# Kernel optimization log

Measured on AMD Instinct MI355X. Metric: run time of the kernel, lower is better.

Reference implementation:

```python
import jax, jax.numpy as jnp
import numpy as np

N_NODES = 100000
N_EDGES = 1700000


def _build_csr(rng, n, e):
    row = rng.integers(0, n, size=e).astype(np.int64)
    col = rng.integers(0, n, size=e).astype(np.int32)
    order = np.argsort(row, kind='stable')
    row = row[order]
    col = col[order]
    rowptr = np.searchsorted(row, np.arange(n + 1)).astype(np.int32)
    return rowptr, col


def setup_inputs() -> dict:
    key = jax.random.key(0)
    k1, k2, k3, k4 = jax.random.split(key, 4)
    rng = np.random.default_rng(0)
    rowptr, colind = _build_csr(rng, N_NODES, N_EDGES)
    F_in, H, C = 256, 128, 16
    return {
        'x': jax.random.normal(k1, (N_NODES, F_in), dtype=jnp.float32),
        'edge_weight': jax.random.uniform(k2, (N_EDGES,), dtype=jnp.float32) + 0.5,
        'W1': jax.random.normal(k3, (F_in, H), dtype=jnp.float32) * (1.0 / np.sqrt(F_in)),
        'b1': jnp.zeros((H,), dtype=jnp.float32),
        'W2': jax.random.normal(k4, (H, C), dtype=jnp.float32) * (1.0 / np.sqrt(H)),
        'b2': jnp.zeros((C,), dtype=jnp.float32),
        'rowptr': jnp.asarray(rowptr),
        'colind': jnp.asarray(colind),
    }


def _rowids_from_rowptr(rowptr, n_edges):
    # CSR rowptr -> per-nnz row index, jit-friendly
    return (jnp.searchsorted(rowptr, jnp.arange(n_edges, dtype=rowptr.dtype), side='right') - 1).astype(jnp.int32)


def reference(x, edge_weight, W1, b1, W2, b2, rowptr, colind):
    n = x.shape[0]
    e = colind.shape[0]
    row = _rowids_from_rowptr(rowptr, e)
    col = colind

    # GCN symmetric normalization: D^-1/2 A D^-1/2 (cached=True -> shared by both layers)
    deg = jax.ops.segment_sum(edge_weight, row, num_segments=n)
    dinv = jnp.where(deg > 0, jax.lax.rsqrt(deg), 0.0)
    w = dinv[row] * edge_weight * dinv[col]

    def gcn_layer(h, W, b):
        h = h @ W                                   # [n, d_out]
        # SpMM: out[r] = sum_e w[e] * h[col[e]]
        msg = w[:, None] * h[col]                   # [e, d_out] gather
        return jax.ops.segment_sum(msg, row, num_segments=n) + b

    h = jax.nn.relu(gcn_layer(x, W1, b1))
    # dropout is identity in eval mode
    out = gcn_layer(h, W2, b2)
    return jax.nn.log_softmax(out, axis=1)
```

## Files before the change

### kernel.cpp

```cpp
#include <hip/hip_runtime.h>
#include <hip/hip_bf16.h>

#define F_IN 256
#define HDIM 128
#define CDIM 16

typedef unsigned short u16;
typedef unsigned int u32;

typedef __attribute__((ext_vector_type(8))) short bf16x8;
typedef __attribute__((ext_vector_type(4))) float f32x4;

__device__ __forceinline__ float bf2f(u32 v) {
    u32 u = v << 16;
    float f;
    __builtin_memcpy(&f, &u, 4);
    return f;
}
__device__ __forceinline__ u16 f2bf(float f) {
    u32 u;
    __builtin_memcpy(&u, &f, 4);
    u32 r = (u + 0x7FFFu + ((u >> 16) & 1u)) >> 16;
    return (u16)r;
}
__device__ __forceinline__ u32 pack2(float lo, float hi) {
    return ((u32)f2bf(hi) << 16) | (u32)f2bf(lo);
}

__global__ void k_dinv(const float* __restrict__ ew, const int* __restrict__ rowptr,
                       float* __restrict__ dinv, int n) {
    int r = blockIdx.x * blockDim.x + threadIdx.x;
    if (r >= n) return;
    int s = rowptr[r], e = rowptr[r + 1];
    float acc = 0.f;
    for (int i = s; i < e; i++) acc += ew[i];
    dinv[r] = (acc > 0.f) ? rsqrtf(acc) : 0.f;
}

__global__ void k_w(const float* __restrict__ ew, const int* __restrict__ rowptr,
                    const int* __restrict__ col, const float* __restrict__ dinv,
                    float* __restrict__ wn, int n) {
    int r = blockIdx.x * blockDim.x + threadIdx.x;
    if (r >= n) return;
    float dr = dinv[r];
    int s = rowptr[r], e = rowptr[r + 1];
    for (int i = s; i < e; i++) wn[i] = dr * ew[i] * dinv[col[i]];
}

__global__ void k_prepw1(const float* __restrict__ W1, u16* __restrict__ W1T) {
    int idx = blockIdx.x * blockDim.x + threadIdx.x;
    if (idx >= HDIM * F_IN) return;
    int f = idx >> 8;
    int k = idx & 255;
    W1T[idx] = f2bf(W1[(size_t)k * HDIM + f]);
}

__global__ __launch_bounds__(512, 4) void k_gemm1(const float* __restrict__ x,
                                                  const u16* __restrict__ W1T,
                                                  u16* __restrict__ T1, int n) {
    __shared__ u16 Bs[HDIM * F_IN];

    int tid = threadIdx.x;
#pragma unroll
    for (int it = 0; it < 8; it++) {
        int o16 = it * 512 + tid;
        u32 o = (u32)o16 * 16;
        u32 swz = o ^ (((o >> 9) & 7u) << 4);
        uint4 v = ((const uint4*)W1T)[o16];
        *(uint4*)((char*)Bs + swz) = v;
    }
    __syncthreads();

    int wave = tid >> 6;
    int lane = tid & 63;
    int lr = lane & 15;
    int kg = lane >> 4;
    int r0 = blockIdx.x * 256 + wave * 32;
    if (r0 >= n) return;

    f32x4 acc[2][8];
#pragma unroll
    for (int rg = 0; rg < 2; rg++)
#pragma unroll
        for (int ct = 0; ct < 8; ct++) acc[rg][ct] = (f32x4){0.f, 0.f, 0.f, 0.f};

    int rowc[2];
#pragma unroll
    for (int rg = 0; rg < 2; rg++) {
        int row = r0 + rg * 16 + lr;
        rowc[rg] = row < n ? row : (n - 1);
    }

#pragma unroll
    for (int kk = 0; kk < F_IN / 32; kk++) {
        bf16x8 afrag[2];
#pragma unroll
        for (int rg = 0; rg < 2; rg++) {
            const float4* ap = (const float4*)(x + (size_t)rowc[rg] * F_IN + kg * 8 + kk * 32);
            float4 alo = ap[0];
            float4 ahi = ap[1];
            afrag[rg][0] = (short)f2bf(alo.x); afrag[rg][1] = (short)f2bf(alo.y);
            afrag[rg][2] = (short)f2bf(alo.z); afrag[rg][3] = (short)f2bf(alo.w);
            afrag[rg][4] = (short)f2bf(ahi.x); afrag[rg][5] = (short)f2bf(ahi.y);
            afrag[rg][6] = (short)f2bf(ahi.z); afrag[rg][7] = (short)f2bf(ahi.w);
        }
#pragma unroll
        for (int ct = 0; ct < 8; ct++) {
            u32 a = (u32)(ct * 16 + lr) * (F_IN * 2) + (u32)kg * 16 + (u32)kk * 64;
            u32 aswz = a ^ (((a >> 9) & 7u) << 4);
            bf16x8 bfrag = *(const bf16x8*)((const char*)Bs + aswz);
#pragma unroll
            for (int rg = 0; rg < 2; rg++)
                acc[rg][ct] = __builtin_amdgcn_mfma_f32_16x16x32_bf16(afrag[rg], bfrag, acc[rg][ct], 0, 0, 0);
        }
    }

#pragma unroll
    for (int rg = 0; rg < 2; rg++) {
        int rbase = r0 + rg * 16 + kg * 4;
#pragma unroll
        for (int ct = 0; ct < 8; ct++) {
#pragma unroll
            for (int i = 0; i < 4; i++) {
                int row = rbase + i;
                if (row < n)
                    T1[(size_t)row * HDIM + ct * 16 + lr] = f2bf(acc[rg][ct][i]);
            }
        }
    }
}

__global__ __launch_bounds__(256) void k_spmm1(const u16* __restrict__ T1,
                                               const float* __restrict__ wn,
                                               const int* __restrict__ rowptr,
                                               const int* __restrict__ col,
                                               const float* __restrict__ b1,
                                               u16* __restrict__ H, int n) {
    int wave = threadIdx.x >> 6;
    int lane = threadIdx.x & 63;
    int r = blockIdx.x * 4 + wave;
    if (r >= n) return;
    int es = lane >> 4;
    int fl = lane & 15;

    int s = rowptr[r], e = rowptr[r + 1];
    float a[8];
#pragma unroll
    for (int j = 0; j < 8; j++) a[j] = 0.f;

    int i = s + es;
    for (; i + 4 < e; i += 8) {
        float w0 = wn[i];
        int c0 = col[i];
        float w1 = wn[i + 4];
        int c1 = col[i + 4];
        uint4 p0 = *(const uint4*)(T1 + (size_t)c0 * HDIM + fl * 8);
        uint4 p1 = *(const uint4*)(T1 + (size_t)c1 * HDIM + fl * 8);
        a[0] += w0 * bf2f(p0.x & 0xFFFFu); a[1] += w0 * bf2f(p0.x >> 16);
        a[2] += w0 * bf2f(p0.y & 0xFFFFu); a[3] += w0 * bf2f(p0.y >> 16);
        a[4] += w0 * bf2f(p0.z & 0xFFFFu); a[5] += w0 * bf2f(p0.z >> 16);
        a[6] += w0 * bf2f(p0.w & 0xFFFFu); a[7] += w0 * bf2f(p0.w >> 16);
        a[0] += w1 * bf2f(p1.x & 0xFFFFu); a[1] += w1 * bf2f(p1.x >> 16);
        a[2] += w1 * bf2f(p1.y & 0xFFFFu); a[3] += w1 * bf2f(p1.y >> 16);
        a[4] += w1 * bf2f(p1.z & 0xFFFFu); a[5] += w1 * bf2f(p1.z >> 16);
        a[6] += w1 * bf2f(p1.w & 0xFFFFu); a[7] += w1 * bf2f(p1.w >> 16);
    }
    if (i < e) {
        float w0 = wn[i];
        int c0 = col[i];
        uint4 p0 = *(const uint4*)(T1 + (size_t)c0 * HDIM + fl * 8);
        a[0] += w0 * bf2f(p0.x & 0xFFFFu); a[1] += w0 * bf2f(p0.x >> 16);
        a[2] += w0 * bf2f(p0.y & 0xFFFFu); a[3] += w0 * bf2f(p0.y >> 16);
        a[4] += w0 * bf2f(p0.z & 0xFFFFu); a[5] += w0 * bf2f(p0.z >> 16);
        a[6] += w0 * bf2f(p0.w & 0xFFFFu); a[7] += w0 * bf2f(p0.w >> 16);
    }

#pragma unroll
    for (int j = 0; j < 8; j++) {
        a[j] += __shfl_xor(a[j], 16);
        a[j] += __shfl_xor(a[j], 32);
    }

    if (es == 0) {
        const float4* bb = (const float4*)(b1 + fl * 8);
        float4 blo = bb[0], bhi = bb[1];
        float v0 = a[0] + blo.x, v1 = a[1] + blo.y;
        float v2 = a[2] + blo.z, v3 = a[3] + blo.w;
        float v4 = a[4] + bhi.x, v5 = a[5] + bhi.y;
        float v6 = a[6] + bhi.z, v7 = a[7] + bhi.w;
        v0 = v0 > 0.f ? v0 : 0.f; v1 = v1 > 0.f ? v1 : 0.f;
        v2 = v2 > 0.f ? v2 : 0.f; v3 = v3 > 0.f ? v3 : 0.f;
        v4 = v4 > 0.f ? v4 : 0.f; v5 = v5 > 0.f ? v5 : 0.f;
        v6 = v6 > 0.f ? v6 : 0.f; v7 = v7 > 0.f ? v7 : 0.f;
        uint4 o;
        o.x = pack2(v0, v1); o.y = pack2(v2, v3);
        o.z = pack2(v4, v5); o.w = pack2(v6, v7);
        *(uint4*)(H + (size_t)r * HDIM + fl * 8) = o;
    }
}

__global__ __launch_bounds__(256) void k_gemm2(const u16* __restrict__ H,
                                               const float* __restrict__ W2,
                                               float* __restrict__ U, int n) {
    int rl = threadIdx.x >> 4;
    int f = threadIdx.x & 15;
    int row = blockIdx.x * 16 + rl;
    if (row >= n) return;
    const u32* hr = (const u32*)(H + (size_t)row * HDIM);
    float acc = 0.f;
    for (int k2 = 0; k2 < HDIM / 2; k2++) {
        u32 pr = hr[k2];
        float h0 = bf2f(pr & 0xFFFFu);
        float h1 = bf2f(pr >> 16);
        acc += h0 * W2[(size_t)(k2 * 2) * CDIM + f];
        acc += h1 * W2[(size_t)(k2 * 2 + 1) * CDIM + f];
    }
    U[(size_t)row * CDIM + f] = acc;
}

__global__ __launch_bounds__(256) void k_out(const float* __restrict__ U,
                                             const float* __restrict__ wn,
                                             const int* __restrict__ rowptr,
                                             const int* __restrict__ col,
                                             const float* __restrict__ b2,
                                             float* __restrict__ out, int n) {
    int wave = threadIdx.x >> 6;
    int lane = threadIdx.x & 63;
    int r = blockIdx.x * 4 + wave;
    if (r >= n) return;
    int es = lane >> 4;
    int f = lane & 15;
    int s = rowptr[r], e = rowptr[r + 1];
    float acc = 0.f;
    int i = s + es;
    for (; i + 4 < e; i += 8) {
        float w0 = wn[i];
        int c0 = col[i];
        float w1 = wn[i + 4];
        int c1 = col[i + 4];
        acc += w0 * U[(size_t)c0 * CDIM + f];
        acc += w1 * U[(size_t)c1 * CDIM + f];
    }
    if (i < e) {
        acc += wn[i] * U[(size_t)col[i] * CDIM + f];
    }
    acc += __shfl_xor(acc, 16);
    acc += __shfl_xor(acc, 32);
    float v = acc + b2[f];
    float m = v;
    for (int d = 1; d < 16; d <<= 1) m = fmaxf(m, __shfl_xor(m, d));
    float ex = __expf(v - m);
    float ss = ex;
    for (int d = 1; d < 16; d <<= 1) ss += __shfl_xor(ss, d);
    float res = v - m - __logf(ss);
    if (es == 0) out[(size_t)r * CDIM + f] = res;
}

extern "C" void kernel_launch(void* const* d_in, const int* in_sizes, int n_in,
                              void* d_out, int out_size, void* d_ws, size_t ws_size,
                              hipStream_t stream) {
    const float* x      = (const float*)d_in[0];
    const float* ew     = (const float*)d_in[1];
    const float* W1     = (const float*)d_in[2];
    const float* b1     = (const float*)d_in[3];
    const float* W2     = (const float*)d_in[4];
    const float* b2     = (const float*)d_in[5];
    const int*   rowptr = (const int*)d_in[6];
    const int*   colind = (const int*)d_in[7];

    int n = in_sizes[6] - 1;
    int E = in_sizes[7];

    auto align256 = [](size_t v) { return (v + 255) & ~(size_t)255; };
    char* p = (char*)d_ws;
    float* dinv = (float*)p; p += align256((size_t)n * 4);
    float* wn   = (float*)p; p += align256((size_t)E * 4);
    u16*   T1   = (u16*)p;   p += align256((size_t)n * HDIM * 2);
    u16*   H    = (u16*)p;   p += align256((size_t)n * HDIM * 2);
    float* U    = (float*)p; p += align256((size_t)n * CDIM * 4);
    u16*   W1T  = (u16*)p;   p += align256((size_t)HDIM * F_IN * 2);
    float* out  = (float*)d_out;

    k_dinv<<<(n + 255) / 256, 256, 0, stream>>>(ew, rowptr, dinv, n);
    k_w<<<(n + 255) / 256, 256, 0, stream>>>(ew, rowptr, colind, dinv, wn, n);
    k_prepw1<<<(HDIM * F_IN + 255) / 256, 256, 0, stream>>>(W1, W1T);

    k_gemm1<<<(n + 255) / 256, 512, 0, stream>>>(x, W1T, T1, n);

    k_spmm1<<<(n + 3) / 4, 256, 0, stream>>>(T1, wn, rowptr, colind, b1, H, n);
    k_gemm2<<<(n + 15) / 16, 256, 0, stream>>>(H, W2, U, n);
    k_out<<<(n + 3) / 4, 256, 0, stream>>>(U, wn, rowptr, colind, b2, out, n);
}
```

Measured before the change: 198.7 us.

## Use packed bf16 convert, deepen SpMM1 unroll, widen k_out gather lanes

Replaces the software fp32-to-bf16 rounding with the hardware v_cvt_pk_bf16_f32 instruction in the GEMM1 A-fragment conversion, the T1 store and the H store. The layer-1 SpMM loop is unrolled to four gathers per lane in flight, to raise memory-level parallelism. The layer-2 gather kernel now assigns 8 edge slots of 8 lanes, each lane loading a float2, so more edges are gathered in parallel per row. The log-softmax reductions are shortened to match. The inline asm depends on the target supporting that instruction, and the deeper unroll raises register use.

```diff
diff --git a/kernel.cpp b/kernel.cpp
--- a/kernel.cpp
+++ b/kernel.cpp
@@ -23,8 +23,10 @@
     u32 r = (u + 0x7FFFu + ((u >> 16) & 1u)) >> 16;
     return (u16)r;
 }
-__device__ __forceinline__ u32 pack2(float lo, float hi) {
-    return ((u32)f2bf(hi) << 16) | (u32)f2bf(lo);
+__device__ __forceinline__ u32 cvtpk(float lo, float hi) {
+    u32 r;
+    asm("v_cvt_pk_bf16_f32 %0, %1, %2" : "=v"(r) : "v"(lo), "v"(hi));
+    return r;
 }
 
 __global__ void k_dinv(const float* __restrict__ ew, const int* __restrict__ rowptr,
@@ -99,10 +101,12 @@
             const float4* ap = (const float4*)(x + (size_t)rowc[rg] * F_IN + kg * 8 + kk * 32);
             float4 alo = ap[0];
             float4 ahi = ap[1];
-            afrag[rg][0] = (short)f2bf(alo.x); afrag[rg][1] = (short)f2bf(alo.y);
-            afrag[rg][2] = (short)f2bf(alo.z); afrag[rg][3] = (short)f2bf(alo.w);
-            afrag[rg][4] = (short)f2bf(ahi.x); afrag[rg][5] = (short)f2bf(ahi.y);
-            afrag[rg][6] = (short)f2bf(ahi.z); afrag[rg][7] = (short)f2bf(ahi.w);
+            u32 q0 = cvtpk(alo.x, alo.y);
+            u32 q1 = cvtpk(alo.z, alo.w);
+            u32 q2 = cvtpk(ahi.x, ahi.y);
+            u32 q3 = cvtpk(ahi.z, ahi.w);
+            u32 qa[4] = {q0, q1, q2, q3};
+            __builtin_memcpy(&afrag[rg], qa, 16);
         }
 #pragma unroll
         for (int ct = 0; ct < 8; ct++) {
@@ -121,10 +125,12 @@
 #pragma unroll
         for (int ct = 0; ct < 8; ct++) {
 #pragma unroll
-            for (int i = 0; i < 4; i++) {
-                int row = rbase + i;
-                if (row < n)
-                    T1[(size_t)row * HDIM + ct * 16 + lr] = f2bf(acc[rg][ct][i]);
+            for (int i = 0; i < 4; i += 2) {
+                u32 q = cvtpk(acc[rg][ct][i], acc[rg][ct][i + 1]);
+                int row0 = rbase + i;
+                int row1 = rbase + i + 1;
+                if (row0 < n) T1[(size_t)row0 * HDIM + ct * 16 + lr] = (u16)(q & 0xFFFFu);
+                if (row1 < n) T1[(size_t)row1 * HDIM + ct * 16 + lr] = (u16)(q >> 16);
             }
         }
     }
@@ -148,32 +154,35 @@
 #pragma unroll
     for (int j = 0; j < 8; j++) a[j] = 0.f;
 
+#define ACCUM(w_, p_) do { \
+        a[0] += (w_) * bf2f((p_).x & 0xFFFFu); a[1] += (w_) * bf2f((p_).x >> 16); \
+        a[2] += (w_) * bf2f((p_).y & 0xFFFFu); a[3] += (w_) * bf2f((p_).y >> 16); \
+        a[4] += (w_) * bf2f((p_).z & 0xFFFFu); a[5] += (w_) * bf2f((p_).z >> 16); \
+        a[6] += (w_) * bf2f((p_).w & 0xFFFFu); a[7] += (w_) * bf2f((p_).w >> 16); \
+    } while (0)
+
     int i = s + es;
-    for (; i + 4 < e; i += 8) {
-        float w0 = wn[i];
-        int c0 = col[i];
-        float w1 = wn[i + 4];
-        int c1 = col[i + 4];
+    for (; i + 12 < e; i += 16) {
+        float w0 = wn[i];      int c0 = col[i];
+        float w1 = wn[i + 4];  int c1 = col[i + 4];
+        float w2 = wn[i + 8];  int c2 = col[i + 8];
+        float w3 = wn[i + 12]; int c3 = col[i + 12];
         uint4 p0 = *(const uint4*)(T1 + (size_t)c0 * HDIM + fl * 8);
         uint4 p1 = *(const uint4*)(T1 + (size_t)c1 * HDIM + fl * 8);
-        a[0] += w0 * bf2f(p0.x & 0xFFFFu); a[1] += w0 * bf2f(p0.x >> 16);
-        a[2] += w0 * bf2f(p0.y & 0xFFFFu); a[3] += w0 * bf2f(p0.y >> 16);
-        a[4] += w0 * bf2f(p0.z & 0xFFFFu); a[5] += w0 * bf2f(p0.z >> 16);
-        a[6] += w0 * bf2f(p0.w & 0xFFFFu); a[7] += w0 * bf2f(p0.w >> 16);
-        a[0] += w1 * bf2f(p1.x & 0xFFFFu); a[1] += w1 * bf2f(p1.x >> 16);
-        a[2] += w1 * bf2f(p1.y & 0xFFFFu); a[3] += w1 * bf2f(p1.y >> 16);
-        a[4] += w1 * bf2f(p1.z & 0xFFFFu); a[5] += w1 * bf2f(p1.z >> 16);
-        a[6] += w1 * bf2f(p1.w & 0xFFFFu); a[7] += w1 * bf2f(p1.w >> 16);
-    }
-    if (i < e) {
+        uint4 p2 = *(const uint4*)(T1 + (size_t)c2 * HDIM + fl * 8);
+        uint4 p3 = *(const uint4*)(T1 + (size_t)c3 * HDIM + fl * 8);
+        ACCUM(w0, p0);
+        ACCUM(w1, p1);
+        ACCUM(w2, p2);
+        ACCUM(w3, p3);
+    }
+    for (; i < e; i += 4) {
         float w0 = wn[i];
         int c0 = col[i];
         uint4 p0 = *(const uint4*)(T1 + (size_t)c0 * HDIM + fl * 8);
-        a[0] += w0 * bf2f(p0.x & 0xFFFFu); a[1] += w0 * bf2f(p0.x >> 16);
-        a[2] += w0 * bf2f(p0.y & 0xFFFFu); a[3] += w0 * bf2f(p0.y >> 16);
-        a[4] += w0 * bf2f(p0.z & 0xFFFFu); a[5] += w0 * bf2f(p0.z >> 16);
-        a[6] += w0 * bf2f(p0.w & 0xFFFFu); a[7] += w0 * bf2f(p0.w >> 16);
-    }
+        ACCUM(w0, p0);
+    }
+#undef ACCUM
 
 #pragma unroll
     for (int j = 0; j < 8; j++) {
@@ -193,8 +202,8 @@
         v4 = v4 > 0.f ? v4 : 0.f; v5 = v5 > 0.f ? v5 : 0.f;
         v6 = v6 > 0.f ? v6 : 0.f; v7 = v7 > 0.f ? v7 : 0.f;
         uint4 o;
-        o.x = pack2(v0, v1); o.y = pack2(v2, v3);
-        o.z = pack2(v4, v5); o.w = pack2(v6, v7);
+        o.x = cvtpk(v0, v1); o.y = cvtpk(v2, v3);
+        o.z = cvtpk(v4, v5); o.w = cvtpk(v6, v7);
         *(uint4*)(H + (size_t)r * HDIM + fl * 8) = o;
     }
 }
@@ -228,32 +237,48 @@
     int lane = threadIdx.x & 63;
     int r = blockIdx.x * 4 + wave;
     if (r >= n) return;
-    int es = lane >> 4;
-    int f = lane & 15;
+    int es = lane >> 3;
+    int fl = lane & 7;
     int s = rowptr[r], e = rowptr[r + 1];
-    float acc = 0.f;
+    float a0 = 0.f, a1 = 0.f;
+
     int i = s + es;
-    for (; i + 4 < e; i += 8) {
+    for (; i + 8 < e; i += 16) {
+        float w0 = wn[i];     int c0 = col[i];
+        float w1 = wn[i + 8]; int c1 = col[i + 8];
+        float2 u0 = *(const float2*)(U + (size_t)c0 * CDIM + fl * 2);
+        float2 u1 = *(const float2*)(U + (size_t)c1 * CDIM + fl * 2);
+        a0 += w0 * u0.x; a1 += w0 * u0.y;
+        a0 += w1 * u1.x; a1 += w1 * u1.y;
+    }
+    for (; i < e; i += 8) {
         float w0 = wn[i];
         int c0 = col[i];
-        float w1 = wn[i + 4];
-        int c1 = col[i + 4];
-        acc += w0 * U[(size_t)c0 * CDIM + f];
-        acc += w1 * U[(size_t)c1 * CDIM + f];
-    }
-    if (i < e) {
-        acc += wn[i] * U[(size_t)col[i] * CDIM + f];
-    }
-    acc += __shfl_xor(acc, 16);
-    acc += __shfl_xor(acc, 32);
-    float v = acc + b2[f];
-    float m = v;
-    for (int d = 1; d < 16; d <<= 1) m = fmaxf(m, __shfl_xor(m, d));
-    float ex = __expf(v - m);
-    float ss = ex;
-    for (int d = 1; d < 16; d <<= 1) ss += __shfl_xor(ss, d);
-    float res = v - m - __logf(ss);
-    if (es == 0) out[(size_t)r * CDIM + f] = res;
+        float2 u0 = *(const float2*)(U + (size_t)c0 * CDIM + fl * 2);
+        a0 += w0 * u0.x; a1 += w0 * u0.y;
+    }
+
+    a0 += __shfl_xor(a0, 8);  a1 += __shfl_xor(a1, 8);
+    a0 += __shfl_xor(a0, 16); a1 += __shfl_xor(a1, 16);
+    a0 += __shfl_xor(a0, 32); a1 += __shfl_xor(a1, 32);
+
+    float2 bp = ((const float2*)b2)[fl];
+    float v0 = a0 + bp.x;
+    float v1 = a1 + bp.y;
+
+    float m = fmaxf(v0, v1);
+    m = fmaxf(m, __shfl_xor(m, 1));
+    m = fmaxf(m, __shfl_xor(m, 2));
+    m = fmaxf(m, __shfl_xor(m, 4));
+    float ss = __expf(v0 - m) + __expf(v1 - m);
+    ss += __shfl_xor(ss, 1);
+    ss += __shfl_xor(ss, 2);
+    ss += __shfl_xor(ss, 4);
+    float ls = __logf(ss);
+    if (es == 0) {
+        float2 res = {v0 - m - ls, v1 - m - ls};
+        *(float2*)(out + (size_t)r * CDIM + fl * 2) = res;
+    }
 }
 
 extern "C" void kernel_launch(void* const* d_in, const int* in_sizes, int n_in,
```

New measurement: 190.5 us. 4.2% less time.
